# Kernel tuning notes

Hardware: AMD Instinct MI355X
Metric: run time of the kernel (lower is better)

Reference implementation:

```python
import jax, jax.numpy as jnp
import numpy as np

D_MODEL = 1024
HEAD = 16
EPS = 1e-6


def _norm(x, alpha, beta):
    # Faithful to NormalizeLayer: torch.std is unbiased (ddof=1); scalar alpha/bias.
    mean = jnp.mean(x, axis=-1, keepdims=True)
    std = jnp.std(x, axis=-1, ddof=1, keepdims=True)
    return alpha * ((x - mean) / (std + EPS)) + beta


def setup_inputs() -> dict:
    key = jax.random.key(0)
    ks = jax.random.split(key, 16)
    B, S, D = 4, 1024, D_MODEL
    s = 1.0 / np.sqrt(D)
    inp = {
        'x': jax.random.normal(ks[0], (B, S, D), dtype=jnp.float32),
        'mask': jnp.ones((B, 1, 1, S), dtype=jnp.int32),
        'Wq_w': jax.random.normal(ks[1], (D, D), dtype=jnp.float32) * s,
        'Wq_b': jnp.zeros((D,), dtype=jnp.float32),
        'Wk_w': jax.random.normal(ks[2], (D, D), dtype=jnp.float32) * s,
        'Wk_b': jnp.zeros((D,), dtype=jnp.float32),
        'Wv_w': jax.random.normal(ks[3], (D, D), dtype=jnp.float32) * s,
        'Wv_b': jnp.zeros((D,), dtype=jnp.float32),
        'Wo_w': jax.random.normal(ks[4], (D, D), dtype=jnp.float32) * s,
        'Wo_b': jnp.zeros((D,), dtype=jnp.float32),
        'ff1_w': jax.random.normal(ks[5], (D, D), dtype=jnp.float32) * s,
        'ff1_b': jnp.zeros((D,), dtype=jnp.float32),
        'ff2_w': jax.random.normal(ks[6], (D, D), dtype=jnp.float32) * s,
        'ff2_b': jnp.zeros((D,), dtype=jnp.float32),
        'alpha1': jnp.ones((1,), dtype=jnp.float32),
        'beta1': jnp.zeros((1,), dtype=jnp.float32),
        'alpha2': jnp.ones((1,), dtype=jnp.float32),
        'beta2': jnp.zeros((1,), dtype=jnp.float32),
    }
    return inp


def reference(x, mask, Wq_w, Wq_b, Wk_w, Wk_b, Wv_w, Wv_b, Wo_w, Wo_b,
              ff1_w, ff1_b, ff2_w, ff2_b, alpha1, beta1, alpha2, beta2):
    B, S, D = x.shape
    H = HEAD
    kd = D // H
    # QKV projections (torch Linear: y = x @ W.T + b)
    Q = (x @ Wq_w.T + Wq_b).reshape(B, S, H, kd).transpose(0, 2, 1, 3)
    K = (x @ Wk_w.T + Wk_b).reshape(B, S, H, kd).transpose(0, 2, 1, 3)
    V = (x @ Wv_w.T + Wv_b).reshape(B, S, H, kd).transpose(0, 2, 1, 3)
    score = jnp.einsum('bhqd,bhkd->bhqk', Q, K) / jnp.sqrt(jnp.float32(kd))
    score = jnp.where(mask == 0, -jnp.inf, score)
    attn = jax.nn.softmax(score, axis=-1)
    o = jnp.einsum('bhqk,bhkd->bhqd', attn, V)
    o = o.transpose(0, 2, 1, 3).reshape(B, S, D)
    attn_out = o @ Wo_w.T + Wo_b
    # residual 1 + custom norm (dropout is identity in eval / drop=0)
    x1 = _norm(x + attn_out, alpha1, beta1)
    # feed-forward: Linear -> ReLU -> Linear (both d_model x d_model)
    ff = jax.nn.relu(x1 @ ff1_w.T + ff1_b) @ ff2_w.T + ff2_b
    # residual 2 + custom norm
    return _norm(x1 + ff, alpha2, beta2)
```

## Files before the change

kernel.cpp:

```cpp
#include <hip/hip_runtime.h>


typedef __bf16 bf16x8 __attribute__((ext_vector_type(8)));
typedef float f32x4 __attribute__((ext_vector_type(4)));
typedef unsigned short ushort4v __attribute__((ext_vector_type(4)));

static __device__ __forceinline__ unsigned short f2bf(float f) {
  return __builtin_bit_cast(unsigned short, (__bf16)f);
}
static __device__ __forceinline__ float bf2f(unsigned short u) {
  return __builtin_bit_cast(float, (unsigned int)u << 16);
}

static __device__ __forceinline__ void gload_lds16(const void* g, void* l) {
  __builtin_amdgcn_global_load_lds(
      (const __attribute__((address_space(1))) unsigned int*)g,
      (__attribute__((address_space(3))) unsigned int*)l, 16, 0, 0);
}

__global__ __launch_bounds__(256)
void cvt_all(const float* __restrict__ x, const float* __restrict__ wq,
             const float* __restrict__ wk, const float* __restrict__ wv,
             const float* __restrict__ wo, const float* __restrict__ w1,
             const float* __restrict__ w2,
             unsigned short* __restrict__ x_bf, unsigned short* __restrict__ wqkv_bf,
             unsigned short* __restrict__ wo_bf, unsigned short* __restrict__ w1_bf,
             unsigned short* __restrict__ w2_bf) {
  const int y = blockIdx.y;
  const size_t MEL = 1u << 20;
  const float* src;
  unsigned short* dst;
  switch (y) {
    case 0: case 1: case 2: case 3: src = x + y * MEL; dst = x_bf + y * MEL; break;
    case 4: src = wq; dst = wqkv_bf; break;
    case 5: src = wk; dst = wqkv_bf + MEL; break;
    case 6: src = wv; dst = wqkv_bf + 2 * MEL; break;
    case 7: src = wo; dst = wo_bf; break;
    case 8: src = w1; dst = w1_bf; break;
    default: src = w2; dst = w2_bf; break;
  }
  const int i = blockIdx.x * 256 + threadIdx.x;
  const float4 v = reinterpret_cast<const float4*>(src)[i];
  ushort4v o;
  o[0] = f2bf(v.x); o[1] = f2bf(v.y); o[2] = f2bf(v.z); o[3] = f2bf(v.w);
  reinterpret_cast<ushort4v*>(dst)[i] = o;
}

template<bool RELU, int OUT_MODE>
__global__ __launch_bounds__(256, 2)
void gemm_bt(const unsigned short* __restrict__ A,
             const unsigned short* __restrict__ W,
             const float* __restrict__ bias0, const float* __restrict__ bias1,
             const float* __restrict__ bias2,
             void* __restrict__ out0, unsigned short* __restrict__ outK,
             unsigned short* __restrict__ outVt, int M, int N, int K) {
  __shared__ __align__(16) unsigned short Al[2][64][64];
  __shared__ __align__(16) unsigned short Bl[2][128][64];
  const int tid = threadIdx.x;
  const int lane = tid & 63;
  const int w = tid >> 6;
  const int wr = w >> 1, wc = w & 1;
  const int grp = lane >> 4, l15 = lane & 15;
  const long bRow = (long)blockIdx.x * 64;
  const long bCol = (long)blockIdx.y * 128;

  f32x4 acc[2][4];
#pragma unroll
  for (int m = 0; m < 2; m++)
#pragma unroll
    for (int n = 0; n < 4; n++) { f32x4 z = {0.f,0.f,0.f,0.f}; acc[m][n] = z; }

  const int srow = tid >> 3;
  const int xc = (((tid & 7) ^ (srow & 7)) << 3);
  const unsigned short* Ag0 = A + (bRow + srow) * (long)K + xc;
  const unsigned short* Ag1 = Ag0 + 32L * K;
  const unsigned short* Wg0 = W + (bCol + srow) * (long)K + xc;
  const unsigned short* Wg1 = Wg0 + 32L * K;
  const unsigned short* Wg2 = Wg0 + 64L * K;
  const unsigned short* Wg3 = Wg0 + 96L * K;

  auto stage = [&](int k0, int buf) {
    unsigned short* ldsA = &Al[buf][0][0] + w * 512;
    unsigned short* ldsB = &Bl[buf][0][0] + w * 512;
    gload_lds16(Ag0 + k0, ldsA);
    gload_lds16(Ag1 + k0, ldsA + 2048);
    gload_lds16(Wg0 + k0, ldsB);
    gload_lds16(Wg1 + k0, ldsB + 2048);
    gload_lds16(Wg2 + k0, ldsB + 4096);
    gload_lds16(Wg3 + k0, ldsB + 6144);
  };

  const int NT = K >> 6;
  stage(0, 0);
  for (int t = 0; t < NT; ++t) {
    const int cur = t & 1;
    __syncthreads();
    if (t + 1 < NT) stage((t + 1) << 6, cur ^ 1);
#pragma unroll
    for (int kk = 0; kk < 2; kk++) {
      bf16x8 af[2], bf[4];
#pragma unroll
      for (int m = 0; m < 2; m++) {
        const int R = wr * 32 + m * 16 + l15;
        const int pos = (kk * 4 + grp) ^ (R & 7);
        af[m] = *(const bf16x8*)&Al[cur][R][pos << 3];
      }
#pragma unroll
      for (int n = 0; n < 4; n++) {
        const int R = wc * 64 + n * 16 + l15;
        const int pos = (kk * 4 + grp) ^ (R & 7);
        bf[n] = *(const bf16x8*)&Bl[cur][R][pos << 3];
      }
#pragma unroll
      for (int m = 0; m < 2; m++)
#pragma unroll
        for (int n = 0; n < 4; n++)
          acc[m][n] = __builtin_amdgcn_mfma_f32_16x16x32_bf16(af[m], bf[n], acc[m][n], 0, 0, 0);
    }
  }

  const int seg = (OUT_MODE == 2) ? (int)(bCol >> 10) : 0;
  const float* bp = (OUT_MODE == 2) ? (seg == 0 ? bias0 : seg == 1 ? bias1 : bias2) : bias0;
#pragma unroll
  for (int n = 0; n < 4; n++) {
    const long col = bCol + wc * 64 + n * 16 + l15;
    const float bv = bp[OUT_MODE == 2 ? (col & 1023) : col];
#pragma unroll
    for (int m = 0; m < 2; m++) {
      const long row0 = bRow + wr * 32 + m * 16 + grp * 4;
#pragma unroll
      for (int r = 0; r < 4; r++) {
        float v = acc[m][n][r] + bv;
        if (RELU) v = fmaxf(v, 0.f);
        const long row = row0 + r;
        if (OUT_MODE == 0) {
          ((float*)out0)[row * (long)N + col] = v;
        } else if (OUT_MODE == 1) {
          ((unsigned short*)out0)[row * (long)N + col] = f2bf(v);
        } else {
          if (seg == 0) {
            ((unsigned short*)out0)[row * 1024 + col] = f2bf(v);
          } else if (seg == 1) {
            outK[row * 1024 + (col & 1023)] = f2bf(v);
          } else {
            const long vc = col & 1023;
            const long idx = (((row >> 10) * 16 + (vc >> 6)) << 16) + ((vc & 63) << 10) + (row & 1023);
            outVt[idx] = f2bf(v);
          }
        }
      }
    }
  }
}

__global__ __launch_bounds__(256)
void attn_kernel(const unsigned short* __restrict__ Qb,
                 const unsigned short* __restrict__ Kb,
                 const unsigned short* __restrict__ Vt_g,
                 const int* __restrict__ maskp,
                 unsigned short* __restrict__ Ob) {
  const int S = 1024, D = 1024;
  __shared__ __align__(16) unsigned short Kl[2][64][64];
  __shared__ __align__(16) unsigned short Vl[2][64][64];
  __shared__ __align__(16) unsigned short Pl[64][64];
  const int tid = threadIdx.x;
  const int lane = tid & 63;
  const int w = tid >> 6;
  const int grp = lane >> 4, l15 = lane & 15;
  const int bh = blockIdx.x;
  const int qt = blockIdx.y;
  const int b = bh >> 4, h = bh & 15;
  const float NEG = -__builtin_inff();
  const float SCL = 0.125f * 1.44269504088896340736f;

  const unsigned short* Qp = Qb + ((size_t)(b * S + qt * 64 + w * 16 + l15)) * D + h * 64;
  const bf16x8 aq0 = *(const bf16x8*)(Qp + grp * 8);
  const bf16x8 aq1 = *(const bf16x8*)(Qp + 32 + grp * 8);

  bf16x8 onesb;
#pragma unroll
  for (int j = 0; j < 8; j++) onesb[j] = (__bf16)1.0f;

  f32x4 acc_o[4];
#pragma unroll
  for (int f = 0; f < 4; f++) { f32x4 z = {0.f,0.f,0.f,0.f}; acc_o[f] = z; }
  f32x4 acc_l = {0.f, 0.f, 0.f, 0.f};
  float M = NEG;

  const int srow = tid >> 3;
  const int xc = (((tid & 7) ^ (srow & 7)) << 3);
  const unsigned short* Kg0 = Kb + ((size_t)(b * S + srow)) * D + h * 64 + xc;
  const unsigned short* Kg1 = Kg0 + 32 * (size_t)D;
  const unsigned short* Vgb = Vt_g + (((size_t)bh) << 16);
  const unsigned short* Vg0 = Vgb + (size_t)srow * S + xc;
  const unsigned short* Vg1 = Vg0 + 32 * (size_t)S;

  auto stage = [&](int kt2, int buf) {
    const size_t kb = (size_t)kt2 * 64;
    gload_lds16(Kg0 + kb * D, &Kl[buf][0][0] + w * 512);
    gload_lds16(Kg1 + kb * D, &Kl[buf][0][0] + w * 512 + 2048);
    gload_lds16(Vg0 + kb,     &Vl[buf][0][0] + w * 512);
    gload_lds16(Vg1 + kb,     &Vl[buf][0][0] + w * 512 + 2048);
  };
  stage(0, 0);

  for (int kt = 0; kt < 16; ++kt) {
    const int cur = kt & 1;
    const int kbase = kt * 64;
    __syncthreads();
    if (kt < 15) stage(kt + 1, cur ^ 1);

    f32x4 sfr[4];
    __builtin_amdgcn_s_setprio(1);
#pragma unroll
    for (int f = 0; f < 4; f++) {
      const int R = f * 16 + l15;
      const int p0 = (grp ^ (R & 7)) << 3;
      const int p1 = ((4 + grp) ^ (R & 7)) << 3;
      bf16x8 bk0 = *(const bf16x8*)&Kl[cur][R][p0];
      bf16x8 bk1 = *(const bf16x8*)&Kl[cur][R][p1];
      f32x4 z = {0.f,0.f,0.f,0.f};
      z = __builtin_amdgcn_mfma_f32_16x16x32_bf16(aq0, bk0, z, 0, 0, 0);
      z = __builtin_amdgcn_mfma_f32_16x16x32_bf16(aq1, bk1, z, 0, 0, 0);
      sfr[f] = z;
    }
    __builtin_amdgcn_s_setprio(0);

#pragma unroll
    for (int f = 0; f < 4; f++) {
      const float biasf = maskp[b * S + kbase + f * 16 + l15] ? 0.f : NEG;
#pragma unroll
      for (int r = 0; r < 4; r++)
        sfr[f][r] = fmaf(sfr[f][r], SCL, biasf);
    }

    float rm = sfr[0][0];
#pragma unroll
    for (int f = 0; f < 4; f++)
#pragma unroll
      for (int r = 0; r < 4; r++) rm = fmaxf(rm, sfr[f][r]);
    rm = fmaxf(rm, __shfl_xor(rm, 1));
    rm = fmaxf(rm, __shfl_xor(rm, 2));
    rm = fmaxf(rm, __shfl_xor(rm, 4));
    rm = fmaxf(rm, __shfl_xor(rm, 8));
    rm = fmaxf(rm, __shfl_xor(rm, 16));
    rm = fmaxf(rm, __shfl_xor(rm, 32));
    if (rm > M + 8.f) {
      const float sc = exp2f(M - rm);
      M = rm;
#pragma unroll
      for (int f = 0; f < 4; f++) acc_o[f] *= sc;
      acc_l *= sc;
    }

#pragma unroll
    for (int f = 0; f < 4; f++) {
#pragma unroll
      for (int r = 0; r < 4; r++) {
        const float p = exp2f(sfr[f][r] - M);
        const int q = w * 16 + grp * 4 + r;
        const int cchunk = (f * 2 + (l15 >> 3)) ^ (q & 7);
        ((unsigned short*)Pl)[q * 64 + (cchunk << 3) + (l15 & 7)] = f2bf(p);
      }
    }

    const int Rp = w * 16 + l15;
    const bf16x8 ap0 = *(const bf16x8*)&Pl[Rp][((grp ^ (Rp & 7)) << 3)];
    const bf16x8 ap1 = *(const bf16x8*)&Pl[Rp][(((4 + grp) ^ (Rp & 7)) << 3)];
    __builtin_amdgcn_s_setprio(1);
#pragma unroll
    for (int f = 0; f < 4; f++) {
      const int Rv = f * 16 + l15;
      bf16x8 bv0 = *(const bf16x8*)&Vl[cur][Rv][((grp ^ (Rv & 7)) << 3)];
      bf16x8 bv1 = *(const bf16x8*)&Vl[cur][Rv][(((4 + grp) ^ (Rv & 7)) << 3)];
      acc_o[f] = __builtin_amdgcn_mfma_f32_16x16x32_bf16(ap0, bv0, acc_o[f], 0, 0, 0);
      acc_o[f] = __builtin_amdgcn_mfma_f32_16x16x32_bf16(ap1, bv1, acc_o[f], 0, 0, 0);
    }
    acc_l = __builtin_amdgcn_mfma_f32_16x16x32_bf16(ap0, onesb, acc_l, 0, 0, 0);
    acc_l = __builtin_amdgcn_mfma_f32_16x16x32_bf16(ap1, onesb, acc_l, 0, 0, 0);
    __builtin_amdgcn_s_setprio(0);
  }

#pragma unroll
  for (int r = 0; r < 4; r++) {
    const float inv = 1.f / acc_l[r];
    const int row = qt * 64 + w * 16 + grp * 4 + r;
#pragma unroll
    for (int f = 0; f < 4; f++) {
      const float v = acc_o[f][r] * inv;
      Ob[((size_t)(b * S + row)) * D + h * 64 + f * 16 + l15] = f2bf(v);
    }
  }
}

template<int AMODE, bool F32OUT, bool BF16OUT>
__global__ __launch_bounds__(256)
void norm_residual(const void* __restrict__ a, const float* __restrict__ bsrc,
                   const float* __restrict__ alpha, const float* __restrict__ beta,
                   float* __restrict__ out, unsigned short* __restrict__ out_bf) {
  const int D = 1024;
  const size_t base = (size_t)blockIdx.x * D + threadIdx.x * 4;
  float a0, a1, a2, a3;
  if (AMODE == 0) {
    const float4 va = *(const float4*)((const float*)a + base);
    a0 = va.x; a1 = va.y; a2 = va.z; a3 = va.w;
  } else {
    const ushort4v va = *(const ushort4v*)((const unsigned short*)a + base);
    a0 = bf2f(va[0]); a1 = bf2f(va[1]); a2 = bf2f(va[2]); a3 = bf2f(va[3]);
  }
  const float4 vb = *(const float4*)(bsrc + base);
  const float x0 = a0 + vb.x, x1 = a1 + vb.y, x2 = a2 + vb.z, x3 = a3 + vb.w;
  float s1 = x0 + x1 + x2 + x3;
  float s2 = x0 * x0 + x1 * x1 + x2 * x2 + x3 * x3;
#pragma unroll
  for (int m = 1; m < 64; m <<= 1) {
    s1 += __shfl_xor(s1, m);
    s2 += __shfl_xor(s2, m);
  }
  __shared__ float red[8];
  const int w = threadIdx.x >> 6, lane = threadIdx.x & 63;
  if (lane == 0) { red[w] = s1; red[4 + w] = s2; }
  __syncthreads();
  s1 = red[0] + red[1] + red[2] + red[3];
  s2 = red[4] + red[5] + red[6] + red[7];
  const float mean = s1 * (1.f / 1024.f);
  const float var = fmaxf((s2 - 1024.f * mean * mean) * (1.f / 1023.f), 0.f);
  const float k = alpha[0] / (sqrtf(var) + 1e-6f);
  const float b0 = beta[0];
  const float y0 = (x0 - mean) * k + b0;
  const float y1 = (x1 - mean) * k + b0;
  const float y2 = (x2 - mean) * k + b0;
  const float y3 = (x3 - mean) * k + b0;
  if (F32OUT) {
    float4 o = {y0, y1, y2, y3};
    *(float4*)(out + base) = o;
  }
  if (BF16OUT) {
    ushort4v ob;
    ob[0] = f2bf(y0); ob[1] = f2bf(y1); ob[2] = f2bf(y2); ob[3] = f2bf(y3);
    *(ushort4v*)(out_bf + base) = ob;
  }
}

extern "C" void kernel_launch(void* const* d_in, const int* in_sizes, int n_in,
                              void* d_out, int out_size, void* d_ws, size_t ws_size,
                              hipStream_t stream) {
  const float* x      = (const float*)d_in[0];
  const int*   maskp  = (const int*)d_in[1];
  const float* Wq_w   = (const float*)d_in[2];
  const float* Wq_b   = (const float*)d_in[3];
  const float* Wk_w   = (const float*)d_in[4];
  const float* Wk_b   = (const float*)d_in[5];
  const float* Wv_w   = (const float*)d_in[6];
  const float* Wv_b   = (const float*)d_in[7];
  const float* Wo_w   = (const float*)d_in[8];
  const float* Wo_b   = (const float*)d_in[9];
  const float* W1_w   = (const float*)d_in[10];
  const float* W1_b   = (const float*)d_in[11];
  const float* W2_w   = (const float*)d_in[12];
  const float* W2_b   = (const float*)d_in[13];
  const float* alpha1 = (const float*)d_in[14];
  const float* beta1  = (const float*)d_in[15];
  const float* alpha2 = (const float*)d_in[16];
  const float* beta2  = (const float*)d_in[17];

  const int B = 4, S = 1024, D = 1024;
  const int M = B * S;
  const size_t MiB = 1u << 20;
  char* ws = (char*)d_ws;
  unsigned short* x_bf    = (unsigned short*)(ws + 0 * MiB);
  unsigned short* Wqkv_bf = (unsigned short*)(ws + 8 * MiB);
  unsigned short* Wo_bf   = (unsigned short*)(ws + 14 * MiB);
  unsigned short* W1_bf   = (unsigned short*)(ws + 16 * MiB);
  unsigned short* W2_bf   = (unsigned short*)(ws + 18 * MiB);
  unsigned short* Q_bf    = (unsigned short*)(ws + 20 * MiB);
  unsigned short* K_bf    = (unsigned short*)(ws + 28 * MiB);
  unsigned short* Vt_bf   = (unsigned short*)(ws + 36 * MiB);
  unsigned short* O_bf    = (unsigned short*)(ws + 44 * MiB);
  float*          attnpr  = (float*)(ws + 52 * MiB);
  unsigned short* x1_bf   = (unsigned short*)(ws + 20 * MiB);
  unsigned short* ff1_bf  = (unsigned short*)(ws + 28 * MiB);
  float*          ff2buf  = (float*)(ws + 36 * MiB);

  cvt_all<<<dim3(1024, 10), dim3(256), 0, stream>>>(
      x, Wq_w, Wk_w, Wv_w, Wo_w, W1_w, W2_w, x_bf, Wqkv_bf, Wo_bf, W1_bf, W2_bf);

  gemm_bt<false, 2><<<dim3(M / 64, 24), dim3(256), 0, stream>>>(
      x_bf, Wqkv_bf, Wq_b, Wk_b, Wv_b, Q_bf, K_bf, Vt_bf, M, 3072, D);

  attn_kernel<<<dim3(B * 16, S / 64), dim3(256), 0, stream>>>(Q_bf, K_bf, Vt_bf, maskp, O_bf);

  gemm_bt<false, 0><<<dim3(M / 64, 8), dim3(256), 0, stream>>>(
      O_bf, Wo_bf, Wo_b, nullptr, nullptr, attnpr, nullptr, nullptr, M, D, D);
  norm_residual<0, false, true><<<dim3(M), dim3(256), 0, stream>>>(
      x, attnpr, alpha1, beta1, nullptr, x1_bf);
  gemm_bt<true, 1><<<dim3(M / 64, 8), dim3(256), 0, stream>>>(
      x1_bf, W1_bf, W1_b, nullptr, nullptr, ff1_bf, nullptr, nullptr, M, D, D);
  gemm_bt<false, 0><<<dim3(M / 64, 8), dim3(256), 0, stream>>>(
      ff1_bf, W2_bf, W2_b, nullptr, nullptr, ff2buf, nullptr, nullptr, M, D, D);
  norm_residual<1, true, false><<<dim3(M), dim3(256), 0, stream>>>(
      x1_bf, ff2buf, alpha2, beta2, (float*)d_out, nullptr);
}
```

Before: 187.8 us.

## Enlarge GEMM tiles, fold Q scale into projection, skip dense mask, bf16 intermediates

The GEMM block tile grows from 64x128 to 128x128, so each wave computes 4x4 MFMA fragments and reuses its staged operand tiles more. The softmax scale moves into the Q projection epilogue, and the attention kernel checks once whether the whole mask is live, skipping the per-tile mask loads when it is. The Wo and FF2 GEMM outputs are written as bf16 instead of fp32, and the residual-norm kernel gains a bf16 input mode to read them. The larger tile doubles LDS and accumulator registers and halves the grid, which may lower occupancy, and bf16 intermediates cost precision.

```diff
diff --git a/kernel.cpp b/kernel.cpp
--- a/kernel.cpp
+++ b/kernel.cpp
@@ -54,40 +54,40 @@
              const float* __restrict__ bias2,
              void* __restrict__ out0, unsigned short* __restrict__ outK,
              unsigned short* __restrict__ outVt, int M, int N, int K) {
-  __shared__ __align__(16) unsigned short Al[2][64][64];
+  __shared__ __align__(16) unsigned short Al[2][128][64];
   __shared__ __align__(16) unsigned short Bl[2][128][64];
   const int tid = threadIdx.x;
   const int lane = tid & 63;
   const int w = tid >> 6;
   const int wr = w >> 1, wc = w & 1;
   const int grp = lane >> 4, l15 = lane & 15;
-  const long bRow = (long)blockIdx.x * 64;
+  const long bRow = (long)blockIdx.x * 128;
   const long bCol = (long)blockIdx.y * 128;
 
-  f32x4 acc[2][4];
-#pragma unroll
-  for (int m = 0; m < 2; m++)
+  f32x4 acc[4][4];
+#pragma unroll
+  for (int m = 0; m < 4; m++)
 #pragma unroll
     for (int n = 0; n < 4; n++) { f32x4 z = {0.f,0.f,0.f,0.f}; acc[m][n] = z; }
 
   const int srow = tid >> 3;
   const int xc = (((tid & 7) ^ (srow & 7)) << 3);
-  const unsigned short* Ag0 = A + (bRow + srow) * (long)K + xc;
-  const unsigned short* Ag1 = Ag0 + 32L * K;
-  const unsigned short* Wg0 = W + (bCol + srow) * (long)K + xc;
-  const unsigned short* Wg1 = Wg0 + 32L * K;
-  const unsigned short* Wg2 = Wg0 + 64L * K;
-  const unsigned short* Wg3 = Wg0 + 96L * K;
+  const unsigned short* Ag[4];
+  const unsigned short* Wg[4];
+#pragma unroll
+  for (int r = 0; r < 4; r++) {
+    Ag[r] = A + (bRow + r * 32 + srow) * (long)K + xc;
+    Wg[r] = W + (bCol + r * 32 + srow) * (long)K + xc;
+  }
 
   auto stage = [&](int k0, int buf) {
     unsigned short* ldsA = &Al[buf][0][0] + w * 512;
     unsigned short* ldsB = &Bl[buf][0][0] + w * 512;
-    gload_lds16(Ag0 + k0, ldsA);
-    gload_lds16(Ag1 + k0, ldsA + 2048);
-    gload_lds16(Wg0 + k0, ldsB);
-    gload_lds16(Wg1 + k0, ldsB + 2048);
-    gload_lds16(Wg2 + k0, ldsB + 4096);
-    gload_lds16(Wg3 + k0, ldsB + 6144);
+#pragma unroll
+    for (int r = 0; r < 4; r++) {
+      gload_lds16(Ag[r] + k0, ldsA + r * 2048);
+      gload_lds16(Wg[r] + k0, ldsB + r * 2048);
+    }
   };
 
   const int NT = K >> 6;
@@ -98,10 +98,10 @@
     if (t + 1 < NT) stage((t + 1) << 6, cur ^ 1);
 #pragma unroll
     for (int kk = 0; kk < 2; kk++) {
-      bf16x8 af[2], bf[4];
-#pragma unroll
-      for (int m = 0; m < 2; m++) {
-        const int R = wr * 32 + m * 16 + l15;
+      bf16x8 af[4], bfr[4];
+#pragma unroll
+      for (int m = 0; m < 4; m++) {
+        const int R = wr * 64 + m * 16 + l15;
         const int pos = (kk * 4 + grp) ^ (R & 7);
         af[m] = *(const bf16x8*)&Al[cur][R][pos << 3];
       }
@@ -109,16 +109,17 @@
       for (int n = 0; n < 4; n++) {
         const int R = wc * 64 + n * 16 + l15;
         const int pos = (kk * 4 + grp) ^ (R & 7);
-        bf[n] = *(const bf16x8*)&Bl[cur][R][pos << 3];
+        bfr[n] = *(const bf16x8*)&Bl[cur][R][pos << 3];
       }
 #pragma unroll
-      for (int m = 0; m < 2; m++)
+      for (int m = 0; m < 4; m++)
 #pragma unroll
         for (int n = 0; n < 4; n++)
-          acc[m][n] = __builtin_amdgcn_mfma_f32_16x16x32_bf16(af[m], bf[n], acc[m][n], 0, 0, 0);
-    }
-  }
-
+          acc[m][n] = __builtin_amdgcn_mfma_f32_16x16x32_bf16(af[m], bfr[n], acc[m][n], 0, 0, 0);
+    }
+  }
+
+  const float QSCL = 0.125f * 1.44269504088896340736f;
   const int seg = (OUT_MODE == 2) ? (int)(bCol >> 10) : 0;
   const float* bp = (OUT_MODE == 2) ? (seg == 0 ? bias0 : seg == 1 ? bias1 : bias2) : bias0;
 #pragma unroll
@@ -126,20 +127,18 @@
     const long col = bCol + wc * 64 + n * 16 + l15;
     const float bv = bp[OUT_MODE == 2 ? (col & 1023) : col];
 #pragma unroll
-    for (int m = 0; m < 2; m++) {
-      const long row0 = bRow + wr * 32 + m * 16 + grp * 4;
+    for (int m = 0; m < 4; m++) {
+      const long row0 = bRow + wr * 64 + m * 16 + grp * 4;
 #pragma unroll
       for (int r = 0; r < 4; r++) {
         float v = acc[m][n][r] + bv;
         if (RELU) v = fmaxf(v, 0.f);
         const long row = row0 + r;
-        if (OUT_MODE == 0) {
-          ((float*)out0)[row * (long)N + col] = v;
-        } else if (OUT_MODE == 1) {
+        if (OUT_MODE == 1) {
           ((unsigned short*)out0)[row * (long)N + col] = f2bf(v);
         } else {
           if (seg == 0) {
-            ((unsigned short*)out0)[row * 1024 + col] = f2bf(v);
+            ((unsigned short*)out0)[row * 1024 + col] = f2bf(v * QSCL);
           } else if (seg == 1) {
             outK[row * 1024 + (col & 1023)] = f2bf(v);
           } else {
@@ -171,7 +170,9 @@
   const int qt = blockIdx.y;
   const int b = bh >> 4, h = bh & 15;
   const float NEG = -__builtin_inff();
-  const float SCL = 0.125f * 1.44269504088896340736f;
+
+  const int4 mv = *(const int4*)(maskp + b * S + tid * 4);
+  const int allLive = __syncthreads_and(mv.x && mv.y && mv.z && mv.w);
 
   const unsigned short* Qp = Qb + ((size_t)(b * S + qt * 64 + w * 16 + l15)) * D + h * 64;
   const bf16x8 aq0 = *(const bf16x8*)(Qp + grp * 8);
@@ -226,19 +227,21 @@
     }
     __builtin_amdgcn_s_setprio(0);
 
-#pragma unroll
-    for (int f = 0; f < 4; f++) {
-      const float biasf = maskp[b * S + kbase + f * 16 + l15] ? 0.f : NEG;
-#pragma unroll
-      for (int r = 0; r < 4; r++)
-        sfr[f][r] = fmaf(sfr[f][r], SCL, biasf);
-    }
-
-    float rm = sfr[0][0];
-#pragma unroll
-    for (int f = 0; f < 4; f++)
-#pragma unroll
-      for (int r = 0; r < 4; r++) rm = fmaxf(rm, sfr[f][r]);
+    if (!allLive) {
+#pragma unroll
+      for (int f = 0; f < 4; f++) {
+        const float biasf = maskp[b * S + kbase + f * 16 + l15] ? 0.f : NEG;
+#pragma unroll
+        for (int r = 0; r < 4; r++) sfr[f][r] += biasf;
+      }
+    }
+
+    float t0 = fmaxf(fmaxf(sfr[0][0], sfr[0][1]), sfr[0][2]);
+    float t1 = fmaxf(fmaxf(sfr[0][3], sfr[1][0]), sfr[1][1]);
+    float t2 = fmaxf(fmaxf(sfr[1][2], sfr[1][3]), sfr[2][0]);
+    float t3 = fmaxf(fmaxf(sfr[2][1], sfr[2][2]), sfr[2][3]);
+    float t4 = fmaxf(fmaxf(sfr[3][0], sfr[3][1]), sfr[3][2]);
+    float rm = fmaxf(fmaxf(fmaxf(t0, t1), t2), fmaxf(fmaxf(t3, t4), sfr[3][3]));
     rm = fmaxf(rm, __shfl_xor(rm, 1));
     rm = fmaxf(rm, __shfl_xor(rm, 2));
     rm = fmaxf(rm, __shfl_xor(rm, 4));
@@ -293,14 +296,14 @@
   }
 }
 
-template<int AMODE, bool F32OUT, bool BF16OUT>
+template<int AMODE, int BMODE, bool F32OUT, bool BF16OUT>
 __global__ __launch_bounds__(256)
-void norm_residual(const void* __restrict__ a, const float* __restrict__ bsrc,
+void norm_residual(const void* __restrict__ a, const void* __restrict__ bsrc,
                    const float* __restrict__ alpha, const float* __restrict__ beta,
                    float* __restrict__ out, unsigned short* __restrict__ out_bf) {
   const int D = 1024;
   const size_t base = (size_t)blockIdx.x * D + threadIdx.x * 4;
-  float a0, a1, a2, a3;
+  float a0, a1, a2, a3, b0v, b1v, b2v, b3v;
   if (AMODE == 0) {
     const float4 va = *(const float4*)((const float*)a + base);
     a0 = va.x; a1 = va.y; a2 = va.z; a3 = va.w;
@@ -308,8 +311,14 @@
     const ushort4v va = *(const ushort4v*)((const unsigned short*)a + base);
     a0 = bf2f(va[0]); a1 = bf2f(va[1]); a2 = bf2f(va[2]); a3 = bf2f(va[3]);
   }
-  const float4 vb = *(const float4*)(bsrc + base);
-  const float x0 = a0 + vb.x, x1 = a1 + vb.y, x2 = a2 + vb.z, x3 = a3 + vb.w;
+  if (BMODE == 0) {
+    const float4 vb = *(const float4*)((const float*)bsrc + base);
+    b0v = vb.x; b1v = vb.y; b2v = vb.z; b3v = vb.w;
+  } else {
+    const ushort4v vb = *(const ushort4v*)((const unsigned short*)bsrc + base);
+    b0v = bf2f(vb[0]); b1v = bf2f(vb[1]); b2v = bf2f(vb[2]); b3v = bf2f(vb[3]);
+  }
+  const float x0 = a0 + b0v, x1 = a1 + b1v, x2 = a2 + b2v, x3 = a3 + b3v;
   float s1 = x0 + x1 + x2 + x3;
   float s2 = x0 * x0 + x1 * x1 + x2 * x2 + x3 * x3;
 #pragma unroll
@@ -377,27 +386,27 @@
   unsigned short* K_bf    = (unsigned short*)(ws + 28 * MiB);
   unsigned short* Vt_bf   = (unsigned short*)(ws + 36 * MiB);
   unsigned short* O_bf    = (unsigned short*)(ws + 44 * MiB);
-  float*          attnpr  = (float*)(ws + 52 * MiB);
+  unsigned short* attn_bf = (unsigned short*)(ws + 52 * MiB);
   unsigned short* x1_bf   = (unsigned short*)(ws + 20 * MiB);
   unsigned short* ff1_bf  = (unsigned short*)(ws + 28 * MiB);
-  float*          ff2buf  = (float*)(ws + 36 * MiB);
+  unsigned short* ff2_bf  = (unsigned short*)(ws + 36 * MiB);
 
   cvt_all<<<dim3(1024, 10), dim3(256), 0, stream>>>(
       x, Wq_w, Wk_w, Wv_w, Wo_w, W1_w, W2_w, x_bf, Wqkv_bf, Wo_bf, W1_bf, W2_bf);
 
-  gemm_bt<false, 2><<<dim3(M / 64, 24), dim3(256), 0, stream>>>(
+  gemm_bt<false, 2><<<dim3(M / 128, 24), dim3(256), 0, stream>>>(
       x_bf, Wqkv_bf, Wq_b, Wk_b, Wv_b, Q_bf, K_bf, Vt_bf, M, 3072, D);
 
   attn_kernel<<<dim3(B * 16, S / 64), dim3(256), 0, stream>>>(Q_bf, K_bf, Vt_bf, maskp, O_bf);
 
-  gemm_bt<false, 0><<<dim3(M / 64, 8), dim3(256), 0, stream>>>(
-      O_bf, Wo_bf, Wo_b, nullptr, nullptr, attnpr, nullptr, nullptr, M, D, D);
-  norm_residual<0, false, true><<<dim3(M), dim3(256), 0, stream>>>(
-      x, attnpr, alpha1, beta1, nullptr, x1_bf);
-  gemm_bt<true, 1><<<dim3(M / 64, 8), dim3(256), 0, stream>>>(
+  gemm_bt<false, 1><<<dim3(M / 128, 8), dim3(256), 0, stream>>>(
+      O_bf, Wo_bf, Wo_b, nullptr, nullptr, attn_bf, nullptr, nullptr, M, D, D);
+  norm_residual<0, 1, false, true><<<dim3(M), dim3(256), 0, stream>>>(
+      x, attn_bf, alpha1, beta1, nullptr, x1_bf);
+  gemm_bt<true, 1><<<dim3(M / 128, 8), dim3(256), 0, stream>>>(
       x1_bf, W1_bf, W1_b, nullptr, nullptr, ff1_bf, nullptr, nullptr, M, D, D);
-  gemm_bt<false, 0><<<dim3(M / 64, 8), dim3(256), 0, stream>>>(
-      ff1_bf, W2_bf, W2_b, nullptr, nullptr, ff2buf, nullptr, nullptr, M, D, D);
-  norm_residual<1, true, false><<<dim3(M), dim3(256), 0, stream>>>(
-      x1_bf, ff2buf, alpha2, beta2, (float*)d_out, nullptr);
-}
+  gemm_bt<false, 1><<<dim3(M / 128, 8), dim3(256), 0, stream>>>(
+      ff1_bf, W2_bf, W2_b, nullptr, nullptr, ff2_bf, nullptr, nullptr, M, D, D);
+  norm_residual<1, 1, true, false><<<dim3(M), dim3(256), 0, stream>>>(
+      x1_bf, ff2_bf, alpha2, beta2, (float*)d_out, nullptr);
+}
```

Measured after the change: 186.9 us. About the same (-0.5%).
